# Optimization experiments

Measured on AMD Instinct MI355X. Metric: run time of the kernel, lower is better.

## Reference

```python
import jax, jax.numpy as jnp
import numpy as np

N_DIRS = 16384
D_MODEL = 1024
BATCH = 4096
K = 32
MULTIK = 128  # min(4*K, N_DIRS)
AUXK = 256
DEAD_STEPS_THRESHOLD = 266


def setup_inputs() -> dict:
    key = jax.random.key(0)
    k1, k2, k3, k4, k5, k6 = jax.random.split(key, 6)
    return {
        "x": jax.random.normal(k1, (BATCH, D_MODEL), dtype=jnp.float32),
        "W_enc": jax.random.normal(k2, (N_DIRS, D_MODEL), dtype=jnp.float32) * 0.02,
        "W_dec": jax.random.normal(k3, (D_MODEL, N_DIRS), dtype=jnp.float32) * 0.02,
        "pre_bias": jax.random.normal(k4, (D_MODEL,), dtype=jnp.float32) * 0.02,
        "latent_bias": jax.random.normal(k5, (N_DIRS,), dtype=jnp.float32) * 0.02,
        "stats_last_nonzero": jax.random.randint(k6, (N_DIRS,), 0, 512, dtype=jnp.int64)
        if jax.config.jax_enable_x64 else
        jax.random.randint(k6, (N_DIRS,), 0, 512, dtype=jnp.int32),
    }


def _scatter_topk(pre, k):
    """top-k on last dim, relu values, scatter into dense zeros (k-sparse SAE)."""
    vals, idx = jax.lax.top_k(pre, k)          # [B, k]
    vals = jax.nn.relu(vals)
    rows = jnp.arange(pre.shape[0])[:, None]   # [B, 1]
    dense = jnp.zeros_like(pre).at[rows, idx].set(vals)
    return vals, idx, dense


def reference(x, W_enc, W_dec, pre_bias, latent_bias, stats_last_nonzero):
    xc = x - pre_bias                                   # [B, d_model]
    latents_pre_act = xc @ W_enc.T + latent_bias        # [B, n_dirs]

    topk_values, topk_indices, latents = _scatter_topk(latents_pre_act, K)
    multik_values, multik_indices, multik_latents = _scatter_topk(latents_pre_act, MULTIK)

    recons = latents @ W_dec.T + pre_bias               # [B, d_model]
    multik_recons = multik_latents @ W_dec.T + pre_bias

    # auxk on dead latents (stats buffer is a constant snapshot here)
    dead_mask = (stats_last_nonzero > DEAD_STEPS_THRESHOLD).astype(latents_pre_act.dtype)
    auxk_values, auxk_indices = jax.lax.top_k(latents_pre_act * dead_mask, AUXK)
    auxk_values = jax.nn.relu(auxk_values)

    return (recons, multik_recons, topk_values, topk_indices,
            auxk_values, auxk_indices, latents_pre_act, latents)
```

## Files before the change

kernel.cpp:

```cpp
#include <hip/hip_runtime.h>
#include <hip/hip_bf16.h>
#include <cstdint>

#define NDIRS 16384
#define DMODEL 1024
#define BATCH 4096
#define KTOP 32
#define MKK 128
#define AUXK 256
#define DEADTHR 266
#define CAND_MAX 2048
#define FOLD_T0 31

__device__ __forceinline__ unsigned fkey(float f) {
  unsigned u = __float_as_uint(f);
  return (u & 0x80000000u) ? ~u : (u | 0x80000000u);
}

__global__ __launch_bounds__(256) void k_transpose(const float* __restrict__ Wdec,
                                                   float* __restrict__ WdT) {
  __shared__ float tile[32][33];
  const int tx = threadIdx.x & 31, ty = threadIdx.x >> 5;
  const int c0 = blockIdx.x * 32;
  const int r0 = blockIdx.y * 32;
#pragma unroll
  for (int i = 0; i < 32; i += 8)
    tile[ty + i][tx] = Wdec[(size_t)(r0 + ty + i) * NDIRS + c0 + tx];
  __syncthreads();
#pragma unroll
  for (int i = 0; i < 32; i += 8)
    WdT[(size_t)(c0 + ty + i) * DMODEL + r0 + tx] = tile[tx][ty + i];
}

__global__ __launch_bounds__(256, 2) void k_gemm_enc(
    const float* __restrict__ x, const float* __restrict__ Wenc,
    const float* __restrict__ pre_bias, const float* __restrict__ lat_bias,
    float* __restrict__ P) {
  __shared__ __align__(16) float As[2][16][132];
  __shared__ __align__(16) float Bs[2][16][132];
  const int t = threadIdx.x;
  const int tx = t & 15, ty = t >> 4;
  const int bn = blockIdx.x;
  const int bm = blockIdx.y;
  const int lr = t >> 2;
  const int lk = (t & 3) << 2;

  const float* xA = x + (size_t)(bm * 128 + lr) * DMODEL;
  const float* wB = Wenc + (size_t)(bn * 128 + lr) * DMODEL;

  float acc[8][8];
#pragma unroll
  for (int i = 0; i < 8; ++i)
#pragma unroll
    for (int j = 0; j < 8; ++j) acc[i][j] = 0.f;

  const int c0 = bn * 128 + tx * 8;
  const int rdA = ty * 8;
  const int rdB = tx * 8;

  float4 pb = *(const float4*)(pre_bias + lk);
  float4 a0 = *(const float4*)(xA + lk);
  float4 a1 = *(const float4*)(xA + (size_t)64 * DMODEL + lk);
  float4 b0 = *(const float4*)(wB + lk);
  float4 b1 = *(const float4*)(wB + (size_t)64 * DMODEL + lk);

  int cur = 0;
  for (int tt = 0; tt < DMODEL / 16; ++tt) {
    As[cur][lk + 0][lr] = a0.x - pb.x;
    As[cur][lk + 1][lr] = a0.y - pb.y;
    As[cur][lk + 2][lr] = a0.z - pb.z;
    As[cur][lk + 3][lr] = a0.w - pb.w;
    As[cur][lk + 0][lr + 64] = a1.x - pb.x;
    As[cur][lk + 1][lr + 64] = a1.y - pb.y;
    As[cur][lk + 2][lr + 64] = a1.z - pb.z;
    As[cur][lk + 3][lr + 64] = a1.w - pb.w;
    Bs[cur][lk + 0][lr] = b0.x;  Bs[cur][lk + 1][lr] = b0.y;
    Bs[cur][lk + 2][lr] = b0.z;  Bs[cur][lk + 3][lr] = b0.w;
    Bs[cur][lk + 0][lr + 64] = b1.x;  Bs[cur][lk + 1][lr + 64] = b1.y;
    Bs[cur][lk + 2][lr + 64] = b1.z;  Bs[cur][lk + 3][lr + 64] = b1.w;
    __syncthreads();
    if (tt < DMODEL / 16 - 1) {
      const int k0 = (tt + 1) * 16;
      pb = *(const float4*)(pre_bias + k0 + lk);
      a0 = *(const float4*)(xA + k0 + lk);
      a1 = *(const float4*)(xA + (size_t)64 * DMODEL + k0 + lk);
      b0 = *(const float4*)(wB + k0 + lk);
      b1 = *(const float4*)(wB + (size_t)64 * DMODEL + k0 + lk);
    }
#pragma unroll
    for (int k = 0; k < 16; ++k) {
      float a[8], b[8];
      *(float4*)&a[0] = *(const float4*)&As[cur][k][rdA];
      *(float4*)&a[4] = *(const float4*)&As[cur][k][rdA + 4];
      *(float4*)&b[0] = *(const float4*)&Bs[cur][k][rdB];
      *(float4*)&b[4] = *(const float4*)&Bs[cur][k][rdB + 4];
#pragma unroll
      for (int i = 0; i < 8; ++i)
#pragma unroll
        for (int j = 0; j < 8; ++j) acc[i][j] = fmaf(a[i], b[j], acc[i][j]);
    }
    if (tt == FOLD_T0) {
#pragma unroll
      for (int i = 0; i < 8; ++i) {
        const size_t ro = (size_t)(bm * 128 + ty * 8 + i) * NDIRS + c0;
        *(float4*)(P + ro) = *(float4*)&acc[i][0];
        *(float4*)(P + ro + 4) = *(float4*)&acc[i][4];
#pragma unroll
        for (int j = 0; j < 8; ++j) acc[i][j] = 0.f;
      }
    }
    cur ^= 1;
  }

  float lb8[8];
  *(float4*)&lb8[0] = *(const float4*)(lat_bias + c0);
  *(float4*)&lb8[4] = *(const float4*)(lat_bias + c0 + 4);
#pragma unroll
  for (int i = 0; i < 8; ++i) {
    const size_t ro = (size_t)(bm * 128 + ty * 8 + i) * NDIRS + c0;
    float p0[8];
    *(float4*)&p0[0] = *(const float4*)(P + ro);
    *(float4*)&p0[4] = *(const float4*)(P + ro + 4);
    float o[8];
#pragma unroll
    for (int j = 0; j < 8; ++j) o[j] = (p0[j] + acc[i][j]) + lb8[j];
    *(float4*)(P + ro) = *(float4*)&o[0];
    *(float4*)(P + ro + 4) = *(float4*)&o[4];
  }
}

template <bool USET>
__global__ __launch_bounds__(256) void k_select_recons(
    const float* __restrict__ P, const int* __restrict__ stats,
    const float* __restrict__ Wd,
    const float* __restrict__ pre_bias,
    float* __restrict__ topk_v, float* __restrict__ topk_i,
    float* __restrict__ auxk_v, float* __restrict__ auxk_i,
    float* __restrict__ latents, float* __restrict__ recons,
    float* __restrict__ mrecons) {
  __shared__ unsigned histA[2048];
  __shared__ unsigned histD[2048];
  __shared__ unsigned chunk[256];
  __shared__ __align__(16) unsigned char uni[32768];
  __shared__ float sv[MKK];
  __shared__ int si[MKK];
  __shared__ unsigned cntA, cntD, sTa, sTd;

  unsigned (*pkA)[1024] = (unsigned(*)[1024])uni;
  unsigned (*pkD)[1024] = (unsigned(*)[1024])(uni + 16384);
  unsigned* candKeyA = (unsigned*)uni;
  unsigned short* candIdxA = (unsigned short*)(uni + 8192);
  unsigned* candKeyD = (unsigned*)(uni + 12288);
  unsigned short* candIdxD = (unsigned short*)(uni + 20480);

  const int t = threadIdx.x;
  const int w = t >> 6;
  const int b = blockIdx.x;
  const float* rp = P + (size_t)b * NDIRS;

  for (int i = t; i < 8192; i += 256) ((unsigned*)uni)[i] = 0;
  if (t == 0) { cntA = 0; cntD = 0; sTa = 0; sTd = 0; }
  __syncthreads();
#pragma unroll
  for (int i = 0; i < 16; ++i) {
    const int e = (i * 256 + t) * 4;
    const float4 v = *(const float4*)(rp + e);
    const int4 s = *(const int4*)(stats + e);
    const float hv[4] = {v.x, v.y, v.z, v.w};
    const int sx[4] = {s.x, s.y, s.z, s.w};
#pragma unroll
    for (int c = 0; c < 4; ++c) {
      const unsigned bin = fkey(hv[c]) >> 21;
      const unsigned inc = 1u << ((bin & 1) << 4);
      atomicAdd(&pkA[w][bin >> 1], inc);
      if (sx[c] > DEADTHR && hv[c] > 0.f) atomicAdd(&pkD[w][bin >> 1], inc);
    }
  }
  __syncthreads();
  for (int i = t; i < 2048; i += 256) {
    const int word = i >> 1, sh = (i & 1) << 4;
    unsigned sa = 0, sd = 0;
#pragma unroll
    for (int q = 0; q < 4; ++q) {
      sa += (pkA[q][word] >> sh) & 0xFFFFu;
      sd += (pkD[q][word] >> sh) & 0xFFFFu;
    }
    histA[i] = sa;
    histD[i] = sd;
  }
  __syncthreads();
  {
    unsigned cs = 0;
#pragma unroll
    for (int j = 0; j < 8; ++j) cs += histA[t * 8 + j];
    chunk[t] = cs;
    __syncthreads();
    for (int s = 1; s < 256; s <<= 1) {
      unsigned add = (t + s < 256) ? chunk[t + s] : 0;
      __syncthreads();
      chunk[t] += add;
      __syncthreads();
    }
    unsigned suf = (t + 1 < 256) ? chunk[t + 1] : 0;
    for (int j = 7; j >= 0; --j) {
      const unsigned h = histA[t * 8 + j];
      const unsigned ab = suf;
      suf += h;
      if (suf >= MKK && ab < MKK) sTa = (unsigned)(t * 8 + j);
    }
  }
  __syncthreads();
  {
    unsigned cs = 0;
#pragma unroll
    for (int j = 0; j < 8; ++j) cs += histD[t * 8 + j];
    chunk[t] = cs;
    __syncthreads();
    for (int s = 1; s < 256; s <<= 1) {
      unsigned add = (t + s < 256) ? chunk[t + s] : 0;
      __syncthreads();
      chunk[t] += add;
      __syncthreads();
    }
    unsigned suf = (t + 1 < 256) ? chunk[t + 1] : 0;
    for (int j = 7; j >= 0; --j) {
      const unsigned h = histD[t * 8 + j];
      const unsigned ab = suf;
      suf += h;
      if (suf >= AUXK && ab < AUXK) sTd = (unsigned)(t * 8 + j);
    }
  }
  __syncthreads();
  {
    const unsigned Ta = sTa, Td = sTd;
#pragma unroll
    for (int i = 0; i < 16; ++i) {
      const int e = (i * 256 + t) * 4;
      const float4 v = *(const float4*)(rp + e);
      const int4 s = *(const int4*)(stats + e);
      const float hv[4] = {v.x, v.y, v.z, v.w};
      const int sx[4] = {s.x, s.y, s.z, s.w};
#pragma unroll
      for (int c = 0; c < 4; ++c) {
        const unsigned k = fkey(hv[c]);
        const unsigned bin = k >> 21;
        if (bin >= Ta) {
          unsigned p = atomicAdd(&cntA, 1u);
          if (p < CAND_MAX) { candKeyA[p] = k; candIdxA[p] = (unsigned short)(e + c); }
        }
        if (sx[c] > DEADTHR && hv[c] > 0.f && bin >= Td) {
          unsigned p = atomicAdd(&cntD, 1u);
          if (p < CAND_MAX) { candKeyD[p] = k; candIdxD[p] = (unsigned short)(e + c); }
        }
      }
    }
  }
  __syncthreads();
  {
    const unsigned C = cntA < CAND_MAX ? cntA : CAND_MAX;
    for (unsigned i = t; i < C; i += 256) {
      const unsigned ki = candKeyA[i];
      const unsigned ii = candIdxA[i];
      unsigned r = 0;
      for (unsigned j = 0; j < C; ++j) {
        const unsigned kj = candKeyA[j];
        r += (unsigned)((kj > ki) | ((kj == ki) & (candIdxA[j] < ii)));
      }
      if (r < MKK) {
        const float vr = fmaxf(rp[ii], 0.f);
        sv[r] = vr;
        si[r] = (int)ii;
        if (r < KTOP) {
          topk_v[b * KTOP + r] = vr;
          topk_i[b * KTOP + r] = (float)ii;
        }
      }
    }
  }
  {
    const unsigned C = cntD < CAND_MAX ? cntD : CAND_MAX;
    for (unsigned i = t; i < C; i += 256) {
      const unsigned ki = candKeyD[i];
      const unsigned ii = candIdxD[i];
      unsigned r = 0;
      for (unsigned j = 0; j < C; ++j) {
        const unsigned kj = candKeyD[j];
        r += (unsigned)((kj > ki) | ((kj == ki) & (candIdxD[j] < ii)));
      }
      if (r < AUXK) {
        auxk_v[b * AUXK + r] = fmaxf(rp[ii], 0.f);
        auxk_i[b * AUXK + r] = (float)ii;
      }
    }
    if (t == 0 && C < AUXK) {
      for (unsigned r = C; r < AUXK; ++r) {
        auxk_v[b * AUXK + r] = 0.f;
        auxk_i[b * AUXK + r] = 0.f;
      }
    }
  }
  __syncthreads();
  float* latRow = latents + (size_t)b * NDIRS;
  const float4 z4 = make_float4(0.f, 0.f, 0.f, 0.f);
#pragma unroll
  for (int i = 0; i < 16; ++i) *(float4*)(latRow + (i * 256 + t) * 4) = z4;
  __syncthreads();
  if (t < KTOP) latRow[si[t]] = sv[t];
  const int d = t * 4;
  float4 acc = *(const float4*)(pre_bias + d);
  if (USET) {
#pragma unroll 4
    for (int i = 0; i < KTOP; ++i) {
      const float v = sv[i];
      const float4 wv = *(const float4*)(Wd + (size_t)si[i] * DMODEL + d);
      acc.x = fmaf(v, wv.x, acc.x);
      acc.y = fmaf(v, wv.y, acc.y);
      acc.z = fmaf(v, wv.z, acc.z);
      acc.w = fmaf(v, wv.w, acc.w);
    }
    *(float4*)(recons + (size_t)b * DMODEL + d) = acc;
#pragma unroll 4
    for (int i = KTOP; i < MKK; ++i) {
      const float v = sv[i];
      const float4 wv = *(const float4*)(Wd + (size_t)si[i] * DMODEL + d);
      acc.x = fmaf(v, wv.x, acc.x);
      acc.y = fmaf(v, wv.y, acc.y);
      acc.z = fmaf(v, wv.z, acc.z);
      acc.w = fmaf(v, wv.w, acc.w);
    }
    *(float4*)(mrecons + (size_t)b * DMODEL + d) = acc;
  } else {
#pragma unroll 2
    for (int i = 0; i < MKK; ++i) {
      const float v = sv[i];
      const int j = si[i];
      acc.x = fmaf(v, Wd[(size_t)(d + 0) * NDIRS + j], acc.x);
      acc.y = fmaf(v, Wd[(size_t)(d + 1) * NDIRS + j], acc.y);
      acc.z = fmaf(v, Wd[(size_t)(d + 2) * NDIRS + j], acc.z);
      acc.w = fmaf(v, Wd[(size_t)(d + 3) * NDIRS + j], acc.w);
      if (i == KTOP - 1) *(float4*)(recons + (size_t)b * DMODEL + d) = acc;
    }
    *(float4*)(mrecons + (size_t)b * DMODEL + d) = acc;
  }
}

extern "C" void kernel_launch(void* const* d_in, const int* in_sizes, int n_in,
                              void* d_out, int out_size, void* d_ws,
                              size_t ws_size, hipStream_t stream) {
  const float* x = (const float*)d_in[0];
  const float* Wenc = (const float*)d_in[1];
  const float* Wdec = (const float*)d_in[2];
  const float* pre_bias = (const float*)d_in[3];
  const float* lat_bias = (const float*)d_in[4];
  const int* stats = (const int*)d_in[5];

  float* out = (float*)d_out;
  float* recons = out;
  float* mrecons = recons + (size_t)BATCH * DMODEL;
  float* topk_v = mrecons + (size_t)BATCH * DMODEL;
  float* topk_i = topk_v + (size_t)BATCH * KTOP;
  float* auxk_v = topk_i + (size_t)BATCH * KTOP;
  float* auxk_i = auxk_v + (size_t)BATCH * AUXK;
  float* P = auxk_i + (size_t)BATCH * AUXK;
  float* latents = P + (size_t)BATCH * NDIRS;

  const size_t wdT_b = (size_t)NDIRS * DMODEL * sizeof(float);
  float* WdT = (float*)d_ws;
  const bool useT = ws_size >= wdT_b;

  if (useT) {
    dim3 g(NDIRS / 32, DMODEL / 32);
    k_transpose<<<g, 256, 0, stream>>>(Wdec, WdT);
  }
  {
    dim3 g(NDIRS / 128, BATCH / 128);
    k_gemm_enc<<<g, 256, 0, stream>>>(x, Wenc, pre_bias, lat_bias, P);
  }
  if (useT)
    k_select_recons<true><<<BATCH, 256, 0, stream>>>(
        P, stats, WdT, pre_bias, topk_v, topk_i, auxk_v, auxk_i, latents,
        recons, mrecons);
  else
    k_select_recons<false><<<BATCH, 256, 0, stream>>>(
        P, stats, Wdec, pre_bias, topk_v, topk_i, auxk_v, auxk_i, latents,
        recons, mrecons);
}
```

Measured before the change: 2.241 ms.

## Move latents zeroing into GEMM epilogue and widen select kernel to 512 threads

Zeroing of the dense latents buffer moves from the selection kernel into the encoder GEMM epilogue, so the select kernel only scatters the top-k values. The select/reconstruction kernel now runs 512 threads per row instead of 256. The 4 histogram partitions are shared by pairs of waves, and the decoder gather uses float2 per thread. This adds write traffic to the GEMM epilogue and leaves half the threads idle during the scans, but is meant to give more parallelism for the candidate ranking and gather.

Result: faster. 2.104 ms (-6.1%).

```diff
diff --git a/kernel.cpp b/kernel.cpp
--- a/kernel.cpp
+++ b/kernel.cpp
@@ -35,7 +35,7 @@
 __global__ __launch_bounds__(256, 2) void k_gemm_enc(
     const float* __restrict__ x, const float* __restrict__ Wenc,
     const float* __restrict__ pre_bias, const float* __restrict__ lat_bias,
-    float* __restrict__ P) {
+    float* __restrict__ P, float* __restrict__ latents_zero) {
   __shared__ __align__(16) float As[2][16][132];
   __shared__ __align__(16) float Bs[2][16][132];
   const int t = threadIdx.x;
@@ -115,6 +115,7 @@
   float lb8[8];
   *(float4*)&lb8[0] = *(const float4*)(lat_bias + c0);
   *(float4*)&lb8[4] = *(const float4*)(lat_bias + c0 + 4);
+  const float4 z4 = make_float4(0.f, 0.f, 0.f, 0.f);
 #pragma unroll
   for (int i = 0; i < 8; ++i) {
     const size_t ro = (size_t)(bm * 128 + ty * 8 + i) * NDIRS + c0;
@@ -126,11 +127,13 @@
     for (int j = 0; j < 8; ++j) o[j] = (p0[j] + acc[i][j]) + lb8[j];
     *(float4*)(P + ro) = *(float4*)&o[0];
     *(float4*)(P + ro + 4) = *(float4*)&o[4];
+    *(float4*)(latents_zero + ro) = z4;
+    *(float4*)(latents_zero + ro + 4) = z4;
   }
 }
 
 template <bool USET>
-__global__ __launch_bounds__(256) void k_select_recons(
+__global__ __launch_bounds__(512) void k_select_recons(
     const float* __restrict__ P, const int* __restrict__ stats,
     const float* __restrict__ Wd,
     const float* __restrict__ pre_bias,
@@ -154,16 +157,16 @@
   unsigned short* candIdxD = (unsigned short*)(uni + 20480);
 
   const int t = threadIdx.x;
-  const int w = t >> 6;
+  const int w = (t >> 6) & 3;
   const int b = blockIdx.x;
   const float* rp = P + (size_t)b * NDIRS;
 
-  for (int i = t; i < 8192; i += 256) ((unsigned*)uni)[i] = 0;
+  for (int i = t; i < 8192; i += 512) ((unsigned*)uni)[i] = 0;
   if (t == 0) { cntA = 0; cntD = 0; sTa = 0; sTd = 0; }
   __syncthreads();
 #pragma unroll
-  for (int i = 0; i < 16; ++i) {
-    const int e = (i * 256 + t) * 4;
+  for (int i = 0; i < 8; ++i) {
+    const int e = (i * 512 + t) * 4;
     const float4 v = *(const float4*)(rp + e);
     const int4 s = *(const int4*)(stats + e);
     const float hv[4] = {v.x, v.y, v.z, v.w};
@@ -177,7 +180,7 @@
     }
   }
   __syncthreads();
-  for (int i = t; i < 2048; i += 256) {
+  for (int i = t; i < 2048; i += 512) {
     const int word = i >> 1, sh = (i & 1) << 4;
     unsigned sa = 0, sd = 0;
 #pragma unroll
@@ -190,52 +193,60 @@
   }
   __syncthreads();
   {
-    unsigned cs = 0;
-#pragma unroll
-    for (int j = 0; j < 8; ++j) cs += histA[t * 8 + j];
-    chunk[t] = cs;
+    if (t < 256) {
+      unsigned cs = 0;
+#pragma unroll
+      for (int j = 0; j < 8; ++j) cs += histA[t * 8 + j];
+      chunk[t] = cs;
+    }
     __syncthreads();
     for (int s = 1; s < 256; s <<= 1) {
-      unsigned add = (t + s < 256) ? chunk[t + s] : 0;
+      unsigned add = (t < 256 && t + s < 256) ? chunk[t + s] : 0;
       __syncthreads();
-      chunk[t] += add;
+      if (t < 256) chunk[t] += add;
       __syncthreads();
     }
-    unsigned suf = (t + 1 < 256) ? chunk[t + 1] : 0;
-    for (int j = 7; j >= 0; --j) {
-      const unsigned h = histA[t * 8 + j];
-      const unsigned ab = suf;
-      suf += h;
-      if (suf >= MKK && ab < MKK) sTa = (unsigned)(t * 8 + j);
-    }
-  }
-  __syncthreads();
-  {
-    unsigned cs = 0;
-#pragma unroll
-    for (int j = 0; j < 8; ++j) cs += histD[t * 8 + j];
-    chunk[t] = cs;
+    if (t < 256) {
+      unsigned suf = (t + 1 < 256) ? chunk[t + 1] : 0;
+      for (int j = 7; j >= 0; --j) {
+        const unsigned h = histA[t * 8 + j];
+        const unsigned ab = suf;
+        suf += h;
+        if (suf >= MKK && ab < MKK) sTa = (unsigned)(t * 8 + j);
+      }
+    }
+  }
+  __syncthreads();
+  {
+    if (t < 256) {
+      unsigned cs = 0;
+#pragma unroll
+      for (int j = 0; j < 8; ++j) cs += histD[t * 8 + j];
+      chunk[t] = cs;
+    }
     __syncthreads();
     for (int s = 1; s < 256; s <<= 1) {
-      unsigned add = (t + s < 256) ? chunk[t + s] : 0;
+      unsigned add = (t < 256 && t + s < 256) ? chunk[t + s] : 0;
       __syncthreads();
-      chunk[t] += add;
+      if (t < 256) chunk[t] += add;
       __syncthreads();
     }
-    unsigned suf = (t + 1 < 256) ? chunk[t + 1] : 0;
-    for (int j = 7; j >= 0; --j) {
-      const unsigned h = histD[t * 8 + j];
-      const unsigned ab = suf;
-      suf += h;
-      if (suf >= AUXK && ab < AUXK) sTd = (unsigned)(t * 8 + j);
+    if (t < 256) {
+      unsigned suf = (t + 1 < 256) ? chunk[t + 1] : 0;
+      for (int j = 7; j >= 0; --j) {
+        const unsigned h = histD[t * 8 + j];
+        const unsigned ab = suf;
+        suf += h;
+        if (suf >= AUXK && ab < AUXK) sTd = (unsigned)(t * 8 + j);
+      }
     }
   }
   __syncthreads();
   {
     const unsigned Ta = sTa, Td = sTd;
 #pragma unroll
-    for (int i = 0; i < 16; ++i) {
-      const int e = (i * 256 + t) * 4;
+    for (int i = 0; i < 8; ++i) {
+      const int e = (i * 512 + t) * 4;
       const float4 v = *(const float4*)(rp + e);
       const int4 s = *(const int4*)(stats + e);
       const float hv[4] = {v.x, v.y, v.z, v.w};
@@ -258,7 +269,7 @@
   __syncthreads();
   {
     const unsigned C = cntA < CAND_MAX ? cntA : CAND_MAX;
-    for (unsigned i = t; i < C; i += 256) {
+    for (unsigned i = t; i < C; i += 512) {
       const unsigned ki = candKeyA[i];
       const unsigned ii = candIdxA[i];
       unsigned r = 0;
@@ -279,7 +290,7 @@
   }
   {
     const unsigned C = cntD < CAND_MAX ? cntD : CAND_MAX;
-    for (unsigned i = t; i < C; i += 256) {
+    for (unsigned i = t; i < C; i += 512) {
       const unsigned ki = candKeyD[i];
       const unsigned ii = candIdxD[i];
       unsigned r = 0;
@@ -300,35 +311,26 @@
     }
   }
   __syncthreads();
-  float* latRow = latents + (size_t)b * NDIRS;
-  const float4 z4 = make_float4(0.f, 0.f, 0.f, 0.f);
-#pragma unroll
-  for (int i = 0; i < 16; ++i) *(float4*)(latRow + (i * 256 + t) * 4) = z4;
-  __syncthreads();
-  if (t < KTOP) latRow[si[t]] = sv[t];
-  const int d = t * 4;
-  float4 acc = *(const float4*)(pre_bias + d);
+  if (t < KTOP) latents[(size_t)b * NDIRS + si[t]] = sv[t];
+  const int d = t * 2;
+  float2 acc = *(const float2*)(pre_bias + d);
   if (USET) {
 #pragma unroll 4
     for (int i = 0; i < KTOP; ++i) {
       const float v = sv[i];
-      const float4 wv = *(const float4*)(Wd + (size_t)si[i] * DMODEL + d);
+      const float2 wv = *(const float2*)(Wd + (size_t)si[i] * DMODEL + d);
       acc.x = fmaf(v, wv.x, acc.x);
       acc.y = fmaf(v, wv.y, acc.y);
-      acc.z = fmaf(v, wv.z, acc.z);
-      acc.w = fmaf(v, wv.w, acc.w);
-    }
-    *(float4*)(recons + (size_t)b * DMODEL + d) = acc;
+    }
+    *(float2*)(recons + (size_t)b * DMODEL + d) = acc;
 #pragma unroll 4
     for (int i = KTOP; i < MKK; ++i) {
       const float v = sv[i];
-      const float4 wv = *(const float4*)(Wd + (size_t)si[i] * DMODEL + d);
+      const float2 wv = *(const float2*)(Wd + (size_t)si[i] * DMODEL + d);
       acc.x = fmaf(v, wv.x, acc.x);
       acc.y = fmaf(v, wv.y, acc.y);
-      acc.z = fmaf(v, wv.z, acc.z);
-      acc.w = fmaf(v, wv.w, acc.w);
-    }
-    *(float4*)(mrecons + (size_t)b * DMODEL + d) = acc;
+    }
+    *(float2*)(mrecons + (size_t)b * DMODEL + d) = acc;
   } else {
 #pragma unroll 2
     for (int i = 0; i < MKK; ++i) {
@@ -336,11 +338,9 @@
       const int j = si[i];
       acc.x = fmaf(v, Wd[(size_t)(d + 0) * NDIRS + j], acc.x);
       acc.y = fmaf(v, Wd[(size_t)(d + 1) * NDIRS + j], acc.y);
-      acc.z = fmaf(v, Wd[(size_t)(d + 2) * NDIRS + j], acc.z);
-      acc.w = fmaf(v, Wd[(size_t)(d + 3) * NDIRS + j], acc.w);
-      if (i == KTOP - 1) *(float4*)(recons + (size_t)b * DMODEL + d) = acc;
-    }
-    *(float4*)(mrecons + (size_t)b * DMODEL + d) = acc;
+      if (i == KTOP - 1) *(float2*)(recons + (size_t)b * DMODEL + d) = acc;
+    }
+    *(float2*)(mrecons + (size_t)b * DMODEL + d) = acc;
   }
 }
 
@@ -374,14 +374,14 @@
   }
   {
     dim3 g(NDIRS / 128, BATCH / 128);
-    k_gemm_enc<<<g, 256, 0, stream>>>(x, Wenc, pre_bias, lat_bias, P);
+    k_gemm_enc<<<g, 256, 0, stream>>>(x, Wenc, pre_bias, lat_bias, P, latents);
   }
   if (useT)
-    k_select_recons<true><<<BATCH, 256, 0, stream>>>(
+    k_select_recons<true><<<BATCH, 512, 0, stream>>>(
         P, stats, WdT, pre_bias, topk_v, topk_i, auxk_v, auxk_i, latents,
         recons, mrecons);
   else
-    k_select_recons<false><<<BATCH, 256, 0, stream>>>(
+    k_select_recons<false><<<BATCH, 512, 0, stream>>>(
         P, stats, Wdec, pre_bias, topk_v, topk_i, auxk_v, auxk_i, latents,
         recons, mrecons);
 }
```
